# Optimization experiments

Hardware: AMD Instinct MI355X
Metric: run time of the kernel (lower is better)

The kernel has to match this reference:

```python
import jax, jax.numpy as jnp
import numpy as np

D_MODEL = 512
N_HEAD = 8
HEAD_SIZE = D_MODEL // N_HEAD
BLOCK = 512
NORM_EPS = 1e-6


def rmsnorm(x, w, eps=NORM_EPS):
    xf = x.astype(jnp.float32)
    y = xf * jax.lax.rsqrt(jnp.mean(xf * xf, axis=-1, keepdims=True) + eps)
    return y.astype(x.dtype) * w


def setup_inputs() -> dict:
    key = jax.random.key(0)
    ks = jax.random.split(key, 16)
    B, T = 8, 512
    s = 0.02
    return {
        "src": jax.random.normal(ks[0], (B, T, D_MODEL), jnp.float32),
        "norm_w": jnp.ones((D_MODEL,), jnp.float32),
        # per-head projections stacked: [H, d_model, head_size]
        "Wq": jax.random.normal(ks[1], (N_HEAD, D_MODEL, HEAD_SIZE), jnp.float32) * s,
        "bq": jnp.zeros((N_HEAD, HEAD_SIZE), jnp.float32),
        "Wk": jax.random.normal(ks[2], (N_HEAD, D_MODEL, HEAD_SIZE), jnp.float32) * s,
        "bk": jnp.zeros((N_HEAD, HEAD_SIZE), jnp.float32),
        "Wv": jax.random.normal(ks[3], (N_HEAD, D_MODEL, HEAD_SIZE), jnp.float32) * s,
        "bv": jnp.zeros((N_HEAD, HEAD_SIZE), jnp.float32),
        # learned relative-position bias per head: [H, block, block, head_size]
        "rel_pos": jax.random.normal(ks[4], (N_HEAD, BLOCK, BLOCK, HEAD_SIZE), jnp.float32) * s,
        "proj_w": jax.random.normal(ks[5], (D_MODEL, D_MODEL), jnp.float32) * s,
        "proj_b": jnp.zeros((D_MODEL,), jnp.float32),
        "ff_w1": jax.random.normal(ks[6], (D_MODEL, 4 * D_MODEL), jnp.float32) * s,
        "ff_b1": jnp.zeros((4 * D_MODEL,), jnp.float32),
        "ff_w2": jax.random.normal(ks[7], (4 * D_MODEL, D_MODEL), jnp.float32) * s,
        "ff_b2": jnp.zeros((D_MODEL,), jnp.float32),
    }


def reference(src, norm_w, Wq, bq, Wk, bk, Wv, bv, rel_pos,
              proj_w, proj_b, ff_w1, ff_b1, ff_w2, ff_b2):
    B, T, C = src.shape
    x = rmsnorm(src, norm_w)

    # per-head projections (vectorized over heads)
    q = jnp.einsum('btd,hdc->bhtc', x, Wq) + bq[None, :, None, :]
    k = jnp.einsum('btd,hdc->bhtc', x, Wk) + bk[None, :, None, :]
    v = jnp.einsum('btd,hdc->bhtc', x, Wv) + bv[None, :, None, :]

    # NOTE faithful quirk: torch code divides by head_size**(-0.5),
    # i.e. multiplies scores by sqrt(head_size).
    scale = jnp.float32(HEAD_SIZE) ** 0.5
    scores = jnp.einsum('bhtc,bhvc->bhtv', q, k) * scale
    rel = jnp.einsum('bhtc,htvc->bhtv', q, rel_pos[:, :T, :T])
    att = jax.nn.softmax(scores + rel, axis=-1)

    out = jnp.einsum('bhtv,bhvc->bhtc', att, v)            # [B,H,T,hs]
    out = out.transpose(0, 2, 1, 3).reshape(B, T, C)        # concat heads
    att_out = out @ proj_w + proj_b

    src_out = x + att_out
    y = rmsnorm(src_out, norm_w)
    h = jax.nn.gelu(y @ ff_w1 + ff_b1, approximate=False)
    ff_out = h @ ff_w2 + ff_b2
    return y + ff_out
```

## Files before the change

kernel.cpp:

```cpp
#include <hip/hip_runtime.h>
#include <hip/hip_bf16.h>

typedef float  f32x4  __attribute__((ext_vector_type(4)));
typedef short  bf16x8 __attribute__((ext_vector_type(8)));

#define EPI_QKV    0
#define EPI_SCORES 1
#define EPI_ATTV   2
#define EPI_PROJ   3
#define EPI_FF1    4
#define EPI_FF2    5

struct GP {
  const __hip_bfloat16* A;
  const __hip_bfloat16* B;
  int M, N, K;
  int ldA, ldB;
  long long batchA, batchB;
  const float *bias, *bias2, *bias3, *resid;
  float *outF;
  __hip_bfloat16 *outB0, *outB2, *outB3;
  float scale;
};

template<int EPI>
__device__ __forceinline__ void epi_store(const GP& p, int z, int gr, int gc, float v) {
  if (gr >= p.M || gc >= p.N) return;
  if constexpr (EPI == EPI_QKV) {
    int b = gr >> 9, t = gr & 511;
    int which = gc >> 9, hc = gc & 511, h = hc >> 6, c = hc & 63;
    size_t qi = (((size_t)(b * 8 + h) * 512 + t) << 6) + c;
    if (which == 0) {
      float val = v + p.bias[hc];
      p.outF[qi]  = val;
      p.outB0[qi] = __float2bfloat16(val);
    } else if (which == 1) {
      float val = v + p.bias2[hc];
      p.outB2[qi] = __float2bfloat16(val);
    } else {
      float val = v + p.bias3[hc];
      p.outB3[(((size_t)(b * 8 + h) * 64 + c) << 9) + t] = __float2bfloat16(val);
    }
  } else if constexpr (EPI == EPI_SCORES) {
    p.outF[(size_t)z * 262144 + (size_t)gr * 512 + gc] = v * p.scale;
  } else if constexpr (EPI == EPI_ATTV) {
    int b = z >> 3, h = z & 7;
    p.outB0[((size_t)(b * 512 + gr)) * 512 + h * 64 + gc] = __float2bfloat16(v);
  } else if constexpr (EPI == EPI_PROJ) {
    size_t o = (size_t)gr * 512 + gc;
    p.outF[o] = v + p.bias[gc] + p.resid[o];
  } else if constexpr (EPI == EPI_FF1) {
    float x = v + p.bias[gc];
    float g = 0.5f * x * (1.0f + erff(x * 0.70710678118f));
    p.outB0[(size_t)gr * 2048 + gc] = __float2bfloat16(g);
  } else {
    size_t o = (size_t)gr * 512 + gc;
    p.outF[o] = v + p.bias[gc] + p.resid[o];
  }
}

template<int EPI>
__global__ __launch_bounds__(256)
void gemm_k(GP p) {
  __shared__ __align__(16) __hip_bfloat16 As[128 * 64];
  __shared__ __align__(16) __hip_bfloat16 Bs[128 * 64];
  const int tid  = threadIdx.x;
  const int lane = tid & 63;
  const int wave = tid >> 6;
  const int wr = wave >> 1, wc = wave & 1;
  const int m0 = blockIdx.y * 128, n0 = blockIdx.x * 128;
  const int z  = blockIdx.z;
  const __hip_bfloat16* A = p.A + (size_t)z * p.batchA;
  const __hip_bfloat16* B = p.B + (size_t)z * p.batchB;

  f32x4 acc[4][4];
#pragma unroll
  for (int i = 0; i < 4; ++i)
#pragma unroll
    for (int j = 0; j < 4; ++j) acc[i][j] = (f32x4){0.f, 0.f, 0.f, 0.f};

  for (int kt = 0; kt < p.K; kt += 64) {
    __syncthreads();
#pragma unroll
    for (int i = 0; i < 4; ++i) {
      int o = i * 256 + tid;
      int row = o >> 3, s = o & 7;
      int ga = m0 + row; if (ga >= p.M) ga = p.M - 1;
      bf16x8 va = *(const bf16x8*)((const char*)A + ((size_t)ga * p.ldA + kt) * 2 + s * 16);
      *(bf16x8*)((char*)As + row * 128 + ((s ^ (row & 7)) * 16)) = va;
      int gb = n0 + row; if (gb >= p.N) gb = p.N - 1;
      bf16x8 vb = *(const bf16x8*)((const char*)B + ((size_t)gb * p.ldB + kt) * 2 + s * 16);
      *(bf16x8*)((char*)Bs + row * 128 + ((s ^ (row & 7)) * 16)) = vb;
    }
    __syncthreads();
#pragma unroll
    for (int kk = 0; kk < 2; ++kk) {
      int sl = kk * 4 + (lane >> 4);
      bf16x8 af[4], bf_[4];
#pragma unroll
      for (int i = 0; i < 4; ++i) {
        int row = wr * 64 + i * 16 + (lane & 15);
        af[i] = *(const bf16x8*)((const char*)As + row * 128 + ((sl ^ (row & 7)) * 16));
      }
#pragma unroll
      for (int j = 0; j < 4; ++j) {
        int row = wc * 64 + j * 16 + (lane & 15);
        bf_[j] = *(const bf16x8*)((const char*)Bs + row * 128 + ((sl ^ (row & 7)) * 16));
      }
#pragma unroll
      for (int i = 0; i < 4; ++i)
#pragma unroll
        for (int j = 0; j < 4; ++j)
          acc[i][j] = __builtin_amdgcn_mfma_f32_16x16x32_bf16(af[i], bf_[j], acc[i][j], 0, 0, 0);
    }
  }
#pragma unroll
  for (int i = 0; i < 4; ++i)
#pragma unroll
    for (int j = 0; j < 4; ++j)
#pragma unroll
      for (int r = 0; r < 4; ++r) {
        int gr = m0 + wr * 64 + i * 16 + ((lane >> 4) << 2) + r;
        int gc = n0 + wc * 64 + j * 16 + (lane & 15);
        epi_store<EPI>(p, z, gr, gc, acc[i][j][r]);
      }
}

__global__ __launch_bounds__(256)
void rmsnorm_k(const float* __restrict__ in, const float* __restrict__ w,
               float* __restrict__ outF, __hip_bfloat16* __restrict__ outB) {
  const int row = blockIdx.x;
  const float* x = in + (size_t)row * 512;
  const int tid = threadIdx.x;
  float a = x[tid], b = x[tid + 256];
  float ss = a * a + b * b;
#pragma unroll
  for (int off = 32; off > 0; off >>= 1) ss += __shfl_down(ss, off);
  __shared__ float red[4];
  if ((tid & 63) == 0) red[tid >> 6] = ss;
  __syncthreads();
  float tot = red[0] + red[1] + red[2] + red[3];
  float sc = rsqrtf(tot * (1.0f / 512.0f) + 1e-6f);
  float y0 = a * sc * w[tid], y1 = b * sc * w[tid + 256];
  size_t o = (size_t)row * 512;
  outF[o + tid] = y0;           outF[o + tid + 256] = y1;
  outB[o + tid] = __float2bfloat16(y0);
  outB[o + tid + 256] = __float2bfloat16(y1);
}

__global__ __launch_bounds__(256)
void rel_softmax_k(const float* __restrict__ qf, const float* __restrict__ rel_pos,
                   const float* __restrict__ scores, __hip_bfloat16* __restrict__ att) {
  const int t = blockIdx.x, h = blockIdx.y;
  __shared__ float qs[512];
  __shared__ float logits[4096];
  const int tid = threadIdx.x;
  for (int i = tid; i < 512; i += 256) {
    int b = i >> 6, c = i & 63;
    qs[i] = qf[(((size_t)(b * 8 + h) * 512 + t) << 6) + c];
  }
  for (int i = tid; i < 4096; i += 256) {
    int b = i >> 9, v = i & 511;
    logits[i] = scores[((size_t)(b * 8 + h) * 512 + t) * 512 + v];
  }
  __syncthreads();
  const int j = tid & 15, g = tid >> 4;
  float4 q4[8];
#pragma unroll
  for (int b = 0; b < 8; ++b) q4[b] = *(const float4*)&qs[b * 64 + j * 4];
  const float* rb = rel_pos + ((size_t)h * 512 + t) * 512 * 64;
  for (int it = 0; it < 32; ++it) {
    int v = it * 16 + g;
    float4 r4 = *(const float4*)&rb[(size_t)v * 64 + j * 4];
    float part[8];
#pragma unroll
    for (int b = 0; b < 8; ++b)
      part[b] = r4.x * q4[b].x + r4.y * q4[b].y + r4.z * q4[b].z + r4.w * q4[b].w;
#pragma unroll
    for (int off = 1; off < 16; off <<= 1)
#pragma unroll
      for (int b = 0; b < 8; ++b) part[b] += __shfl_xor(part[b], off);
    if (j < 8) logits[j * 512 + v] += part[j];
  }
  __syncthreads();
  const int wave = tid >> 6, lane = tid & 63;
  for (int b = wave; b < 8; b += 4) {
    float vals[8]; float mx = -3.0e38f;
#pragma unroll
    for (int i2 = 0; i2 < 8; ++i2) { vals[i2] = logits[b * 512 + i2 * 64 + lane]; mx = fmaxf(mx, vals[i2]); }
#pragma unroll
    for (int off = 32; off > 0; off >>= 1) mx = fmaxf(mx, __shfl_xor(mx, off));
    float s = 0.f;
#pragma unroll
    for (int i2 = 0; i2 < 8; ++i2) { vals[i2] = __expf(vals[i2] - mx); s += vals[i2]; }
#pragma unroll
    for (int off = 32; off > 0; off >>= 1) s += __shfl_xor(s, off);
    float inv = 1.0f / s;
    __hip_bfloat16* o = att + ((size_t)(b * 8 + h) * 512 + t) * 512;
#pragma unroll
    for (int i2 = 0; i2 < 8; ++i2) o[i2 * 64 + lane] = __float2bfloat16(vals[i2] * inv);
  }
}

__global__ __launch_bounds__(256)
void pack_qkv_w(const float* __restrict__ Wq, const float* __restrict__ Wk,
                const float* __restrict__ Wv, __hip_bfloat16* __restrict__ out) {
  int idx = blockIdx.x * 256 + threadIdx.x;
  if (idx >= 1536 * 512) return;
  int ncol = idx >> 9, d = idx & 511;
  int s = ncol >> 9, hc = ncol & 511, h = hc >> 6, c = hc & 63;
  const float* W = (s == 0) ? Wq : (s == 1) ? Wk : Wv;
  out[idx] = __float2bfloat16(W[((size_t)(h * 512 + d) << 6) + c]);
}

__global__ __launch_bounds__(256)
void transpose_bf16_k(const float* __restrict__ in, __hip_bfloat16* __restrict__ out,
                      int kshift, int Nd, int total) {
  int idx = blockIdx.x * 256 + threadIdx.x;
  if (idx >= total) return;
  int n = idx >> kshift, k = idx & ((1 << kshift) - 1);
  out[idx] = __float2bfloat16(in[(size_t)k * Nd + n]);
}

enum : size_t {
  OFF_XF   = 0,
  OFF_XB   = 8388608,
  OFF_QF   = OFF_XB + 4194304,
  OFF_QB   = OFF_QF + 8388608,
  OFF_KB   = OFF_QB + 4194304,
  OFF_VT   = OFF_KB + 4194304,
  OFF_WQKV = OFF_VT + 4194304,
  OFF_PWT  = OFF_WQKV + 1572864,
  OFF_F1T  = OFF_PWT + 524288,
  OFF_F2T  = OFF_F1T + 2097152,
  OFF_SC   = OFF_F2T + 2097152,
  OFF_ATT  = OFF_SC + 67108864,
  OFF_CAT  = OFF_ATT + 33554432,
  OFF_SO   = OFF_CAT + 4194304,
  OFF_YF   = OFF_SO + 8388608,
  OFF_YB   = OFF_YF + 8388608,
  OFF_H    = OFF_YB + 4194304,
  WS_NEED  = OFF_H + 16777216
};

extern "C" void kernel_launch(void* const* d_in, const int* in_sizes, int n_in,
                              void* d_out, int out_size, void* d_ws, size_t ws_size,
                              hipStream_t stream) {
  const float* src   = (const float*)d_in[0];
  const float* normw = (const float*)d_in[1];
  const float* Wq    = (const float*)d_in[2];
  const float* bq    = (const float*)d_in[3];
  const float* Wk    = (const float*)d_in[4];
  const float* bk    = (const float*)d_in[5];
  const float* Wv    = (const float*)d_in[6];
  const float* bv    = (const float*)d_in[7];
  const float* relp  = (const float*)d_in[8];
  const float* pw    = (const float*)d_in[9];
  const float* pb    = (const float*)d_in[10];
  const float* f1w   = (const float*)d_in[11];
  const float* f1b   = (const float*)d_in[12];
  const float* f2w   = (const float*)d_in[13];
  const float* f2b   = (const float*)d_in[14];
  float* out = (float*)d_out;
  char* ws = (char*)d_ws;

  float*          xf    = (float*)(ws + OFF_XF);
  __hip_bfloat16* xb    = (__hip_bfloat16*)(ws + OFF_XB);
  float*          qf    = (float*)(ws + OFF_QF);
  __hip_bfloat16* qb    = (__hip_bfloat16*)(ws + OFF_QB);
  __hip_bfloat16* kb    = (__hip_bfloat16*)(ws + OFF_KB);
  __hip_bfloat16* vT    = (__hip_bfloat16*)(ws + OFF_VT);
  __hip_bfloat16* wqkvb = (__hip_bfloat16*)(ws + OFF_WQKV);
  __hip_bfloat16* pwt   = (__hip_bfloat16*)(ws + OFF_PWT);
  __hip_bfloat16* f1t   = (__hip_bfloat16*)(ws + OFF_F1T);
  __hip_bfloat16* f2t   = (__hip_bfloat16*)(ws + OFF_F2T);
  float*          sc    = (float*)(ws + OFF_SC);
  __hip_bfloat16* attb  = (__hip_bfloat16*)(ws + OFF_ATT);
  __hip_bfloat16* catb  = (__hip_bfloat16*)(ws + OFF_CAT);
  float*          so    = (float*)(ws + OFF_SO);
  float*          yf    = (float*)(ws + OFF_YF);
  __hip_bfloat16* yb    = (__hip_bfloat16*)(ws + OFF_YB);
  __hip_bfloat16* hb    = (__hip_bfloat16*)(ws + OFF_H);

  pack_qkv_w<<<3072, 256, 0, stream>>>(Wq, Wk, Wv, wqkvb);
  transpose_bf16_k<<<1024, 256, 0, stream>>>(pw,  pwt, 9, 512,  262144);
  transpose_bf16_k<<<4096, 256, 0, stream>>>(f1w, f1t, 9, 2048, 1048576);
  transpose_bf16_k<<<4096, 256, 0, stream>>>(f2w, f2t, 11, 512, 1048576);

  rmsnorm_k<<<4096, 256, 0, stream>>>(src, normw, xf, xb);

  {
    GP p{}; p.A = xb; p.B = wqkvb; p.M = 4096; p.N = 1536; p.K = 512;
    p.ldA = 512; p.ldB = 512; p.batchA = 0; p.batchB = 0;
    p.bias = bq; p.bias2 = bk; p.bias3 = bv;
    p.outF = qf; p.outB0 = qb; p.outB2 = kb; p.outB3 = vT;
    gemm_k<EPI_QKV><<<dim3(12, 32, 1), 256, 0, stream>>>(p);
  }
  {
    GP p{}; p.A = qb; p.B = kb; p.M = 512; p.N = 512; p.K = 64;
    p.ldA = 64; p.ldB = 64; p.batchA = 32768; p.batchB = 32768;
    p.outF = sc; p.scale = 8.0f;
    gemm_k<EPI_SCORES><<<dim3(4, 4, 64), 256, 0, stream>>>(p);
  }
  rel_softmax_k<<<dim3(512, 8), 256, 0, stream>>>(qf, relp, sc, attb);

  {
    GP p{}; p.A = attb; p.B = vT; p.M = 512; p.N = 64; p.K = 512;
    p.ldA = 512; p.ldB = 512; p.batchA = 262144; p.batchB = 32768;
    p.outB0 = catb;
    gemm_k<EPI_ATTV><<<dim3(1, 4, 64), 256, 0, stream>>>(p);
  }
  {
    GP p{}; p.A = catb; p.B = pwt; p.M = 4096; p.N = 512; p.K = 512;
    p.ldA = 512; p.ldB = 512; p.bias = pb; p.resid = xf; p.outF = so;
    gemm_k<EPI_PROJ><<<dim3(4, 32, 1), 256, 0, stream>>>(p);
  }
  rmsnorm_k<<<4096, 256, 0, stream>>>(so, normw, yf, yb);

  {
    GP p{}; p.A = yb; p.B = f1t; p.M = 4096; p.N = 2048; p.K = 512;
    p.ldA = 512; p.ldB = 512; p.bias = f1b; p.outB0 = hb;
    gemm_k<EPI_FF1><<<dim3(16, 32, 1), 256, 0, stream>>>(p);
  }
  {
    GP p{}; p.A = hb; p.B = f2t; p.M = 4096; p.N = 512; p.K = 2048;
    p.ldA = 2048; p.ldB = 2048; p.bias = f2b; p.resid = yf; p.outF = out;
    gemm_k<EPI_FF2><<<dim3(4, 32, 1), 256, 0, stream>>>(p);
  }
}
```

Baseline: 1.024 ms.

## Use MFMA for rel-pos logits, templated GEMM tiles, tiled weight transposes

Result: faster. 874.6 us (-14.6%).

```diff
diff --git a/kernel.cpp b/kernel.cpp
--- a/kernel.cpp
+++ b/kernel.cpp
@@ -3,6 +3,17 @@
 
 typedef float  f32x4  __attribute__((ext_vector_type(4)));
 typedef short  bf16x8 __attribute__((ext_vector_type(8)));
+
+__device__ __forceinline__ short f2bf(float x) {
+  __hip_bfloat16 h = __float2bfloat16(x);
+  return *reinterpret_cast<short*>(&h);
+}
+__device__ __forceinline__ bf16x8 cvt8(float4 a, float4 b) {
+  bf16x8 r;
+  r[0] = f2bf(a.x); r[1] = f2bf(a.y); r[2] = f2bf(a.z); r[3] = f2bf(a.w);
+  r[4] = f2bf(b.x); r[5] = f2bf(b.y); r[6] = f2bf(b.z); r[7] = f2bf(b.w);
+  return r;
+}
 
 #define EPI_QKV    0
 #define EPI_SCORES 1
@@ -25,22 +36,14 @@
 
 template<int EPI>
 __device__ __forceinline__ void epi_store(const GP& p, int z, int gr, int gc, float v) {
-  if (gr >= p.M || gc >= p.N) return;
   if constexpr (EPI == EPI_QKV) {
     int b = gr >> 9, t = gr & 511;
     int which = gc >> 9, hc = gc & 511, h = hc >> 6, c = hc & 63;
     size_t qi = (((size_t)(b * 8 + h) * 512 + t) << 6) + c;
-    if (which == 0) {
-      float val = v + p.bias[hc];
-      p.outF[qi]  = val;
-      p.outB0[qi] = __float2bfloat16(val);
-    } else if (which == 1) {
-      float val = v + p.bias2[hc];
-      p.outB2[qi] = __float2bfloat16(val);
-    } else {
-      float val = v + p.bias3[hc];
-      p.outB3[(((size_t)(b * 8 + h) * 64 + c) << 9) + t] = __float2bfloat16(val);
-    }
+    if (which == 0)      p.outB0[qi] = __float2bfloat16(v + p.bias[hc]);
+    else if (which == 1) p.outB2[qi] = __float2bfloat16(v + p.bias2[hc]);
+    else p.outB3[(((size_t)(b * 8 + h) * 64 + c) << 9) + t] =
+           __float2bfloat16(v + p.bias3[hc]);
   } else if constexpr (EPI == EPI_SCORES) {
     p.outF[(size_t)z * 262144 + (size_t)gr * 512 + gc] = v * p.scale;
   } else if constexpr (EPI == EPI_ATTV) {
@@ -59,69 +62,71 @@
   }
 }
 
-template<int EPI>
+template<int EPI, int BM, int BN>
 __global__ __launch_bounds__(256)
 void gemm_k(GP p) {
-  __shared__ __align__(16) __hip_bfloat16 As[128 * 64];
-  __shared__ __align__(16) __hip_bfloat16 Bs[128 * 64];
+  constexpr int MI = BM / 32, NI = BN / 32;
+  __shared__ __align__(16) __hip_bfloat16 As[BM * 64];
+  __shared__ __align__(16) __hip_bfloat16 Bs[BN * 64];
   const int tid  = threadIdx.x;
   const int lane = tid & 63;
   const int wave = tid >> 6;
   const int wr = wave >> 1, wc = wave & 1;
-  const int m0 = blockIdx.y * 128, n0 = blockIdx.x * 128;
+  const int m0 = blockIdx.y * BM, n0 = blockIdx.x * BN;
   const int z  = blockIdx.z;
   const __hip_bfloat16* A = p.A + (size_t)z * p.batchA;
   const __hip_bfloat16* B = p.B + (size_t)z * p.batchB;
 
-  f32x4 acc[4][4];
-#pragma unroll
-  for (int i = 0; i < 4; ++i)
-#pragma unroll
-    for (int j = 0; j < 4; ++j) acc[i][j] = (f32x4){0.f, 0.f, 0.f, 0.f};
+  f32x4 acc[MI][NI];
+#pragma unroll
+  for (int i = 0; i < MI; ++i)
+#pragma unroll
+    for (int j = 0; j < NI; ++j) acc[i][j] = (f32x4){0.f, 0.f, 0.f, 0.f};
 
   for (int kt = 0; kt < p.K; kt += 64) {
     __syncthreads();
 #pragma unroll
-    for (int i = 0; i < 4; ++i) {
-      int o = i * 256 + tid;
-      int row = o >> 3, s = o & 7;
-      int ga = m0 + row; if (ga >= p.M) ga = p.M - 1;
-      bf16x8 va = *(const bf16x8*)((const char*)A + ((size_t)ga * p.ldA + kt) * 2 + s * 16);
+    for (int i = 0; i < BM / 32; ++i) {
+      int o = i * 256 + tid, row = o >> 3, s = o & 7;
+      bf16x8 va = *(const bf16x8*)((const char*)A + ((size_t)(m0 + row) * p.ldA + kt) * 2 + s * 16);
       *(bf16x8*)((char*)As + row * 128 + ((s ^ (row & 7)) * 16)) = va;
-      int gb = n0 + row; if (gb >= p.N) gb = p.N - 1;
-      bf16x8 vb = *(const bf16x8*)((const char*)B + ((size_t)gb * p.ldB + kt) * 2 + s * 16);
+    }
+#pragma unroll
+    for (int i = 0; i < BN / 32; ++i) {
+      int o = i * 256 + tid, row = o >> 3, s = o & 7;
+      bf16x8 vb = *(const bf16x8*)((const char*)B + ((size_t)(n0 + row) * p.ldB + kt) * 2 + s * 16);
       *(bf16x8*)((char*)Bs + row * 128 + ((s ^ (row & 7)) * 16)) = vb;
     }
     __syncthreads();
 #pragma unroll
     for (int kk = 0; kk < 2; ++kk) {
       int sl = kk * 4 + (lane >> 4);
-      bf16x8 af[4], bf_[4];
-#pragma unroll
-      for (int i = 0; i < 4; ++i) {
-        int row = wr * 64 + i * 16 + (lane & 15);
+      bf16x8 af[MI], bfr[NI];
+#pragma unroll
+      for (int i = 0; i < MI; ++i) {
+        int row = wr * (BM / 2) + i * 16 + (lane & 15);
         af[i] = *(const bf16x8*)((const char*)As + row * 128 + ((sl ^ (row & 7)) * 16));
       }
 #pragma unroll
-      for (int j = 0; j < 4; ++j) {
-        int row = wc * 64 + j * 16 + (lane & 15);
-        bf_[j] = *(const bf16x8*)((const char*)Bs + row * 128 + ((sl ^ (row & 7)) * 16));
+      for (int j = 0; j < NI; ++j) {
+        int row = wc * (BN / 2) + j * 16 + (lane & 15);
+        bfr[j] = *(const bf16x8*)((const char*)Bs + row * 128 + ((sl ^ (row & 7)) * 16));
       }
 #pragma unroll
-      for (int i = 0; i < 4; ++i)
-#pragma unroll
-        for (int j = 0; j < 4; ++j)
-          acc[i][j] = __builtin_amdgcn_mfma_f32_16x16x32_bf16(af[i], bf_[j], acc[i][j], 0, 0, 0);
+      for (int i = 0; i < MI; ++i)
+#pragma unroll
+        for (int j = 0; j < NI; ++j)
+          acc[i][j] = __builtin_amdgcn_mfma_f32_16x16x32_bf16(af[i], bfr[j], acc[i][j], 0, 0, 0);
     }
   }
 #pragma unroll
-  for (int i = 0; i < 4; ++i)
-#pragma unroll
-    for (int j = 0; j < 4; ++j)
+  for (int i = 0; i < MI; ++i)
+#pragma unroll
+    for (int j = 0; j < NI; ++j)
 #pragma unroll
       for (int r = 0; r < 4; ++r) {
-        int gr = m0 + wr * 64 + i * 16 + ((lane >> 4) << 2) + r;
-        int gc = n0 + wc * 64 + j * 16 + (lane & 15);
+        int gr = m0 + wr * (BM / 2) + i * 16 + ((lane >> 4) << 2) + r;
+        int gc = n0 + wc * (BN / 2) + j * 16 + (lane & 15);
         epi_store<EPI>(p, z, gr, gc, acc[i][j][r]);
       }
 }
@@ -149,45 +154,46 @@
 }
 
 __global__ __launch_bounds__(256)
-void rel_softmax_k(const float* __restrict__ qf, const float* __restrict__ rel_pos,
+void rel_softmax_k(const __hip_bfloat16* __restrict__ qb, const float* __restrict__ rel_pos,
                    const float* __restrict__ scores, __hip_bfloat16* __restrict__ att) {
   const int t = blockIdx.x, h = blockIdx.y;
-  __shared__ float qs[512];
-  __shared__ float logits[4096];
-  const int tid = threadIdx.x;
-  for (int i = tid; i < 512; i += 256) {
-    int b = i >> 6, c = i & 63;
-    qs[i] = qf[(((size_t)(b * 8 + h) * 512 + t) << 6) + c];
-  }
-  for (int i = tid; i < 4096; i += 256) {
-    int b = i >> 9, v = i & 511;
-    logits[i] = scores[((size_t)(b * 8 + h) * 512 + t) * 512 + v];
+  __shared__ float logits[8 * 520];
+  const int tid = threadIdx.x, lane = tid & 63, wave = tid >> 6;
+  const int bb = lane & 15, hi = lane >> 4;
+
+  bf16x8 qfrag0, qfrag1;
+  if (bb < 8) {
+    const __hip_bfloat16* qptr = qb + (((size_t)(bb * 8 + h) * 512 + t) << 6);
+    qfrag0 = *(const bf16x8*)(qptr + hi * 8);
+    qfrag1 = *(const bf16x8*)(qptr + 32 + hi * 8);
+  } else {
+    qfrag0 = (bf16x8){0,0,0,0,0,0,0,0};
+    qfrag1 = (bf16x8){0,0,0,0,0,0,0,0};
+  }
+  const float* rb = rel_pos + ((size_t)h * 512 + t) * 512 * 64;
+  const float* sb = scores + (((size_t)((bb & 7) * 8 + h) * 512 + t) << 9);
+
+#pragma unroll
+  for (int mi = 0; mi < 8; ++mi) {
+    int m = wave * 8 + mi;
+    int vb = m * 16 + hi * 4;
+    f32x4 acc = (f32x4){0.f, 0.f, 0.f, 0.f};
+    if (bb < 8) acc = *(const f32x4*)(sb + vb);
+    int vr = m * 16 + bb;
+    const float* ar = rb + (size_t)vr * 64 + hi * 8;
+    float4 a0 = *(const float4*)ar,        a1 = *(const float4*)(ar + 4);
+    float4 a2 = *(const float4*)(ar + 32), a3 = *(const float4*)(ar + 36);
+    bf16x8 af0 = cvt8(a0, a1), af1 = cvt8(a2, a3);
+    acc = __builtin_amdgcn_mfma_f32_16x16x32_bf16(af0, qfrag0, acc, 0, 0, 0);
+    acc = __builtin_amdgcn_mfma_f32_16x16x32_bf16(af1, qfrag1, acc, 0, 0, 0);
+    if (bb < 8) *(f32x4*)&logits[bb * 520 + vb] = acc;
   }
   __syncthreads();
-  const int j = tid & 15, g = tid >> 4;
-  float4 q4[8];
-#pragma unroll
-  for (int b = 0; b < 8; ++b) q4[b] = *(const float4*)&qs[b * 64 + j * 4];
-  const float* rb = rel_pos + ((size_t)h * 512 + t) * 512 * 64;
-  for (int it = 0; it < 32; ++it) {
-    int v = it * 16 + g;
-    float4 r4 = *(const float4*)&rb[(size_t)v * 64 + j * 4];
-    float part[8];
-#pragma unroll
-    for (int b = 0; b < 8; ++b)
-      part[b] = r4.x * q4[b].x + r4.y * q4[b].y + r4.z * q4[b].z + r4.w * q4[b].w;
-#pragma unroll
-    for (int off = 1; off < 16; off <<= 1)
-#pragma unroll
-      for (int b = 0; b < 8; ++b) part[b] += __shfl_xor(part[b], off);
-    if (j < 8) logits[j * 512 + v] += part[j];
-  }
-  __syncthreads();
-  const int wave = tid >> 6, lane = tid & 63;
+
   for (int b = wave; b < 8; b += 4) {
     float vals[8]; float mx = -3.0e38f;
 #pragma unroll
-    for (int i2 = 0; i2 < 8; ++i2) { vals[i2] = logits[b * 512 + i2 * 64 + lane]; mx = fmaxf(mx, vals[i2]); }
+    for (int i2 = 0; i2 < 8; ++i2) { vals[i2] = logits[b * 520 + i2 * 64 + lane]; mx = fmaxf(mx, vals[i2]); }
 #pragma unroll
     for (int off = 32; off > 0; off >>= 1) mx = fmaxf(mx, __shfl_xor(mx, off));
     float s = 0.f;
@@ -203,30 +209,42 @@
 }
 
 __global__ __launch_bounds__(256)
+void transpose_bf16_k(const float* __restrict__ in, __hip_bfloat16* __restrict__ out,
+                      int K, int N) {
+  __shared__ float tile[32][33];
+  const int tx = threadIdx.x & 31, ty = threadIdx.x >> 5;
+  const int n0 = blockIdx.x * 32, k0 = blockIdx.y * 32;
+#pragma unroll
+  for (int i = 0; i < 4; ++i)
+    tile[ty + i * 8][tx] = in[(size_t)(k0 + ty + i * 8) * N + n0 + tx];
+  __syncthreads();
+#pragma unroll
+  for (int i = 0; i < 4; ++i)
+    out[(size_t)(n0 + ty + i * 8) * K + k0 + tx] = __float2bfloat16(tile[tx][ty + i * 8]);
+}
+
+__global__ __launch_bounds__(256)
 void pack_qkv_w(const float* __restrict__ Wq, const float* __restrict__ Wk,
                 const float* __restrict__ Wv, __hip_bfloat16* __restrict__ out) {
-  int idx = blockIdx.x * 256 + threadIdx.x;
-  if (idx >= 1536 * 512) return;
-  int ncol = idx >> 9, d = idx & 511;
-  int s = ncol >> 9, hc = ncol & 511, h = hc >> 6, c = hc & 63;
-  const float* W = (s == 0) ? Wq : (s == 1) ? Wk : Wv;
-  out[idx] = __float2bfloat16(W[((size_t)(h * 512 + d) << 6) + c]);
-}
-
-__global__ __launch_bounds__(256)
-void transpose_bf16_k(const float* __restrict__ in, __hip_bfloat16* __restrict__ out,
-                      int kshift, int Nd, int total) {
-  int idx = blockIdx.x * 256 + threadIdx.x;
-  if (idx >= total) return;
-  int n = idx >> kshift, k = idx & ((1 << kshift) - 1);
-  out[idx] = __float2bfloat16(in[(size_t)k * Nd + n]);
+  __shared__ float tile[32][33];
+  const int s = blockIdx.z >> 3, h = blockIdx.z & 7;
+  const float* W = ((s == 0) ? Wq : (s == 1) ? Wk : Wv) + (size_t)h * 512 * 64;
+  const int tx = threadIdx.x & 31, ty = threadIdx.x >> 5;
+  const int c0 = blockIdx.x * 32, d0 = blockIdx.y * 32;
+#pragma unroll
+  for (int i = 0; i < 4; ++i)
+    tile[ty + i * 8][tx] = W[(size_t)(d0 + ty + i * 8) * 64 + c0 + tx];
+  __syncthreads();
+#pragma unroll
+  for (int i = 0; i < 4; ++i)
+    out[(size_t)s * 262144 + (size_t)(h * 64 + c0 + ty + i * 8) * 512 + d0 + tx] =
+        __float2bfloat16(tile[tx][ty + i * 8]);
 }
 
 enum : size_t {
   OFF_XF   = 0,
   OFF_XB   = 8388608,
-  OFF_QF   = OFF_XB + 4194304,
-  OFF_QB   = OFF_QF + 8388608,
+  OFF_QB   = OFF_XB + 4194304,
   OFF_KB   = OFF_QB + 4194304,
   OFF_VT   = OFF_KB + 4194304,
   OFF_WQKV = OFF_VT + 4194304,
@@ -239,8 +257,7 @@
   OFF_SO   = OFF_CAT + 4194304,
   OFF_YF   = OFF_SO + 8388608,
   OFF_YB   = OFF_YF + 8388608,
-  OFF_H    = OFF_YB + 4194304,
-  WS_NEED  = OFF_H + 16777216
+  OFF_H    = OFF_YB + 4194304
 };
 
 extern "C" void kernel_launch(void* const* d_in, const int* in_sizes, int n_in,
@@ -266,7 +283,6 @@
 
   float*          xf    = (float*)(ws + OFF_XF);
   __hip_bfloat16* xb    = (__hip_bfloat16*)(ws + OFF_XB);
-  float*          qf    = (float*)(ws + OFF_QF);
   __hip_bfloat16* qb    = (__hip_bfloat16*)(ws + OFF_QB);
   __hip_bfloat16* kb    = (__hip_bfloat16*)(ws + OFF_KB);
   __hip_bfloat16* vT    = (__hip_bfloat16*)(ws + OFF_VT);
@@ -282,49 +298,49 @@
   __hip_bfloat16* yb    = (__hip_bfloat16*)(ws + OFF_YB);
   __hip_bfloat16* hb    = (__hip_bfloat16*)(ws + OFF_H);
 
-  pack_qkv_w<<<3072, 256, 0, stream>>>(Wq, Wk, Wv, wqkvb);
-  transpose_bf16_k<<<1024, 256, 0, stream>>>(pw,  pwt, 9, 512,  262144);
-  transpose_bf16_k<<<4096, 256, 0, stream>>>(f1w, f1t, 9, 2048, 1048576);
-  transpose_bf16_k<<<4096, 256, 0, stream>>>(f2w, f2t, 11, 512, 1048576);
+  pack_qkv_w<<<dim3(2, 16, 24), 256, 0, stream>>>(Wq, Wk, Wv, wqkvb);
+  transpose_bf16_k<<<dim3(16, 16), 256, 0, stream>>>(pw,  pwt, 512, 512);
+  transpose_bf16_k<<<dim3(64, 16), 256, 0, stream>>>(f1w, f1t, 512, 2048);
+  transpose_bf16_k<<<dim3(16, 64), 256, 0, stream>>>(f2w, f2t, 2048, 512);
 
   rmsnorm_k<<<4096, 256, 0, stream>>>(src, normw, xf, xb);
 
   {
     GP p{}; p.A = xb; p.B = wqkvb; p.M = 4096; p.N = 1536; p.K = 512;
-    p.ldA = 512; p.ldB = 512; p.batchA = 0; p.batchB = 0;
+    p.ldA = 512; p.ldB = 512;
     p.bias = bq; p.bias2 = bk; p.bias3 = bv;
-    p.outF = qf; p.outB0 = qb; p.outB2 = kb; p.outB3 = vT;
-    gemm_k<EPI_QKV><<<dim3(12, 32, 1), 256, 0, stream>>>(p);
+    p.outB0 = qb; p.outB2 = kb; p.outB3 = vT;
+    gemm_k<EPI_QKV, 64, 128><<<dim3(12, 64, 1), 256, 0, stream>>>(p);
   }
   {
     GP p{}; p.A = qb; p.B = kb; p.M = 512; p.N = 512; p.K = 64;
     p.ldA = 64; p.ldB = 64; p.batchA = 32768; p.batchB = 32768;
     p.outF = sc; p.scale = 8.0f;
-    gemm_k<EPI_SCORES><<<dim3(4, 4, 64), 256, 0, stream>>>(p);
-  }
-  rel_softmax_k<<<dim3(512, 8), 256, 0, stream>>>(qf, relp, sc, attb);
+    gemm_k<EPI_SCORES, 128, 128><<<dim3(4, 4, 64), 256, 0, stream>>>(p);
+  }
+  rel_softmax_k<<<dim3(512, 8), 256, 0, stream>>>(qb, relp, sc, attb);
 
   {
     GP p{}; p.A = attb; p.B = vT; p.M = 512; p.N = 64; p.K = 512;
     p.ldA = 512; p.ldB = 512; p.batchA = 262144; p.batchB = 32768;
     p.outB0 = catb;
-    gemm_k<EPI_ATTV><<<dim3(1, 4, 64), 256, 0, stream>>>(p);
+    gemm_k<EPI_ATTV, 64, 64><<<dim3(1, 8, 64), 256, 0, stream>>>(p);
   }
   {
     GP p{}; p.A = catb; p.B = pwt; p.M = 4096; p.N = 512; p.K = 512;
     p.ldA = 512; p.ldB = 512; p.bias = pb; p.resid = xf; p.outF = so;
-    gemm_k<EPI_PROJ><<<dim3(4, 32, 1), 256, 0, stream>>>(p);
+    gemm_k<EPI_PROJ, 64, 64><<<dim3(8, 64, 1), 256, 0, stream>>>(p);
   }
   rmsnorm_k<<<4096, 256, 0, stream>>>(so, normw, yf, yb);
 
   {
     GP p{}; p.A = yb; p.B = f1t; p.M = 4096; p.N = 2048; p.K = 512;
     p.ldA = 512; p.ldB = 512; p.bias = f1b; p.outB0 = hb;
-    gemm_k<EPI_FF1><<<dim3(16, 32, 1), 256, 0, stream>>>(p);
+    gemm_k<EPI_FF1, 128, 128><<<dim3(16, 32, 1), 256, 0, stream>>>(p);
   }
   {
     GP p{}; p.A = hb; p.B = f2t; p.M = 4096; p.N = 512; p.K = 2048;
     p.ldA = 2048; p.ldB = 2048; p.bias = f2b; p.resid = yf; p.outF = out;
-    gemm_k<EPI_FF2><<<dim3(4, 32, 1), 256, 0, stream>>>(p);
-  }
-}
+    gemm_k<EPI_FF2, 64, 64><<<dim3(8, 64, 1), 256, 0, stream>>>(p);
+  }
+}
```
